# Kernel tuning notes

Hardware: AMD Instinct MI355X
Metric: run time of the kernel (lower is better)

Reference implementation:

```python
import jax, jax.numpy as jnp
import numpy as np

B, N, D = 2, 2048, 1024
H = 16
HD = D // H
C = 4
INTERACTION_BOOST = 0.3
EPS = 1e-6


def _rmsnorm(t, w):
    # t: (B,H,N,HD), w: (HD,)
    var = jnp.mean(t * t, axis=-1, keepdims=True)
    return t * jax.lax.rsqrt(var + EPS) * w


def setup_inputs() -> dict:
    key = jax.random.key(0)
    ks = jax.random.split(key, 8)
    return {
        "x": jax.random.normal(ks[0], (B, N, D), dtype=jnp.float32),
        "character_masks": jax.random.uniform(ks[1], (B, C, N), dtype=jnp.float32),
        "interaction_mask": jax.random.uniform(ks[2], (B, N, N), dtype=jnp.float32),
        "W_qkv": jax.random.normal(ks[3], (3 * D, D), dtype=jnp.float32) * 0.02,
        "W_out": jax.random.normal(ks[4], (D, D), dtype=jnp.float32) * 0.02,
        "q_norm_w": jnp.ones((HD,), dtype=jnp.float32),
        "k_norm_w": jnp.ones((HD,), dtype=jnp.float32),
        "isolation_gate": jax.random.uniform(ks[5], (H,), dtype=jnp.float32),
    }


def reference(x, character_masks, interaction_mask, W_qkv, W_out,
              q_norm_w, k_norm_w, isolation_gate) -> jnp.ndarray:
    b, n, d = x.shape
    h, hd = isolation_gate.shape[0], d // isolation_gate.shape[0]

    qkv = x @ W_qkv.T                       # (B,N,3D)
    q, k, v = jnp.split(qkv, 3, axis=-1)
    def to_heads(t):
        return t.reshape(b, n, h, hd).transpose(0, 2, 1, 3)  # (B,H,N,HD)
    q, k, v = to_heads(q), to_heads(k), to_heads(v)

    q = _rmsnorm(q, q_norm_w)
    k = _rmsnorm(k, k_norm_w)

    scale = hd ** -0.5
    attn = jnp.einsum('bhqd,bhkd->bhqk', q, k) * scale   # (B,H,N,N)

    # isolation bias: same-character co-membership, row-max normalized
    same = jnp.einsum('bcq,bck->bqk', character_masks, character_masks)  # (B,N,N)
    same = same / jnp.clip(jnp.max(same, axis=-1, keepdims=True), 1e-6)
    bias = (same - 0.5) * 2.0 + INTERACTION_BOOST * interaction_mask     # (B,N,N)

    gate = jnp.clip(isolation_gate, 0.0, 1.0)[None, :, None, None]       # (1,H,1,1)
    attn = attn + gate * bias[:, None, :, :] * 3.0

    attn = jax.nn.softmax(attn, axis=-1)
    out = jnp.einsum('bhqk,bhkd->bhqd', attn, v)          # (B,H,N,HD)
    out = out.transpose(0, 2, 1, 3).reshape(b, n, d)      # (B,N,D)
    return out @ W_out.T
```

## Files before the change

### kernel.cpp

```cpp
#include <hip/hip_runtime.h>
#include <math.h>


typedef __attribute__((ext_vector_type(8))) short s8v;
typedef __attribute__((ext_vector_type(4))) short s4v;
typedef __attribute__((ext_vector_type(4))) float f4v;

#define L2E 1.44269504088896340736f

__device__ __forceinline__ unsigned short f2bf(float x) {
    union { float f; unsigned u; } v; v.f = x;
    unsigned r = v.u + 0x7FFF + ((v.u >> 16) & 1);
    return (unsigned short)(r >> 16);
}
__device__ __forceinline__ float bf2f(unsigned short h) {
    union { unsigned u; float f; } v; v.u = ((unsigned)h) << 16;
    return v.f;
}
__device__ __forceinline__ f4v mfma32(s8v a, s8v b, f4v c) {
    return __builtin_amdgcn_mfma_f32_16x16x32_bf16(a, b, c, 0, 0, 0);
}
__device__ __forceinline__ void gl_lds16(const void* g, void* l) {
    __builtin_amdgcn_global_load_lds(
        (const __attribute__((address_space(1))) unsigned*)g,
        (__attribute__((address_space(3))) unsigned*)l, 16, 0, 0);
}
__device__ __forceinline__ float exp2g(float x) {
    float r; asm("v_exp_f32 %0, %1" : "=v"(r) : "v"(x)); return r;
}

__global__ __launch_bounds__(256)
void planes_k(const float* __restrict__ src, short* __restrict__ ph,
              short* __restrict__ pl)
{
    const int i = blockIdx.x * 256 + threadIdx.x;
    float4 f = ((const float4*)src)[i];
    float fa[4] = {f.x, f.y, f.z, f.w};
    s4v h4, l4;
#pragma unroll
    for (int j = 0; j < 4; j++) {
        unsigned short hb = f2bf(fa[j]);
        h4[j] = (short)hb;
        l4[j] = (short)f2bf(fa[j] - bf2f(hb));
    }
    ((s4v*)ph)[i] = h4;
    ((s4v*)pl)[i] = l4;
}

template<int MODE, int NT>
__global__ __launch_bounds__(512, 2)
void gemm2(const short* __restrict__ Ah, const short* __restrict__ Al,
           const short* __restrict__ Bh, const short* __restrict__ Bl,
           short* __restrict__ Qhp, short* __restrict__ Qlp,
           short* __restrict__ Khp, short* __restrict__ Klp,
           short* __restrict__ Vp, float* __restrict__ Cout,
           const float* __restrict__ qw, const float* __restrict__ kw)
{
    extern __shared__ short L[];
    short* sAh = L;
    short* sAl = L + 8192;
    short* sBh = L + 16384;
    short* sBl = L + 24576;

    const int t = threadIdx.x, w = t >> 6, lane = t & 63;
    const int col = lane & 15, quad = lane >> 4;
    const int wm = w >> 1;
    const int wn = w & 1;

    const int srow = t >> 2;
    const int sko  = ((t & 3) ^ (srow & 3)) * 8;
    const int sdst = t * 8;

    int tid = blockIdx.x;
    int m0 = (tid & 31) * 128, n0 = (tid >> 5) * 128;
    const short* agh = Ah + (size_t)(m0 + srow)*1024 + sko;
    const short* agl = Al + (size_t)(m0 + srow)*1024 + sko;
    const short* bgh = Bh + (size_t)(n0 + srow)*1024 + sko;
    const short* bgl = Bl + (size_t)(n0 + srow)*1024 + sko;

    auto stage = [&](int k0, int pp) {
        gl_lds16(agh + k0, &sAh[pp*4096 + sdst]);
        gl_lds16(agl + k0, &sAl[pp*4096 + sdst]);
        gl_lds16(bgh + k0, &sBh[pp*4096 + sdst]);
        gl_lds16(bgl + k0, &sBl[pp*4096 + sdst]);
    };
    stage(0, 0);

    for (int rep = 0; rep < NT; rep++) {
        __syncthreads();

        f4v acc[2][4];
#pragma unroll
        for (int i = 0; i < 2; i++)
#pragma unroll
            for (int j = 0; j < 4; j++) { f4v z = {0.f,0.f,0.f,0.f}; acc[i][j] = z; }

        for (int kt = 0; kt < 32; kt++) {
            const int pp = kt & 1;
            if (kt < 31) stage((kt + 1) * 32, pp ^ 1);

            const int swz = ((quad ^ (col & 3)) << 3);
            s8v bhf[4], blf[4];
#pragma unroll
            for (int j = 0; j < 4; j++) {
                const int boff = pp*4096 + (wn*64 + j*16 + col)*32 + swz;
                bhf[j] = *(const s8v*)&sBh[boff];
                blf[j] = *(const s8v*)&sBl[boff];
            }
#pragma unroll
            for (int i = 0; i < 2; i++) {
                const int aoff = pp*4096 + (wm*32 + i*16 + col)*32 + swz;
                s8v ah = *(const s8v*)&sAh[aoff];
                s8v al = *(const s8v*)&sAl[aoff];
#pragma unroll
                for (int j = 0; j < 4; j++) {
                    acc[i][j] = mfma32(ah, bhf[j], acc[i][j]);
                    acc[i][j] = mfma32(ah, blf[j], acc[i][j]);
                    acc[i][j] = mfma32(al, bhf[j], acc[i][j]);
                }
            }
            __syncthreads();
        }

        const int em0 = m0, en0 = n0;
        if (rep + 1 < NT) {
            tid = blockIdx.x + (rep + 1) * 256;
            m0 = (tid & 31) * 128; n0 = (tid >> 5) * 128;
            agh = Ah + (size_t)(m0 + srow)*1024 + sko;
            agl = Al + (size_t)(m0 + srow)*1024 + sko;
            bgh = Bh + (size_t)(n0 + srow)*1024 + sko;
            bgl = Bl + (size_t)(n0 + srow)*1024 + sko;
            stage(0, 0);
        }

        if (MODE == 0) {
            const int whichW = (en0 + wn*64) >> 10;
            if (whichW < 2) {
                const float* nw = (whichW == 0) ? qw : kw;
                const float sfac = (whichW == 0) ? (0.125f * L2E) : 1.0f;
                float wj[4];
#pragma unroll
                for (int j = 0; j < 4; j++) wj[j] = nw[j*16 + col] * sfac;
#pragma unroll
                for (int i = 0; i < 2; i++)
#pragma unroll
                for (int r = 0; r < 4; r++) {
                    float s2 = acc[i][0][r]*acc[i][0][r] + acc[i][1][r]*acc[i][1][r]
                             + acc[i][2][r]*acc[i][2][r] + acc[i][3][r]*acc[i][3][r];
                    s2 += __shfl_xor(s2, 1);
                    s2 += __shfl_xor(s2, 2);
                    s2 += __shfl_xor(s2, 4);
                    s2 += __shfl_xor(s2, 8);
                    const float scn = rsqrtf(s2*(1.0f/64.0f) + 1e-6f);
#pragma unroll
                    for (int j = 0; j < 4; j++) acc[i][j][r] *= scn*wj[j];
                }
            }
#pragma unroll
            for (int i = 0; i < 2; i++)
#pragma unroll
            for (int j = 0; j < 4; j++) {
                const int gcol = en0 + wn*64 + j*16 + col;
                const int which = gcol >> 10;
                const int hh = (gcol >> 6) & 15;
                const int hd = gcol & 63;
                const int grow0 = em0 + wm*32 + i*16 + quad*4;
                const int b = grow0 >> 11, nn0 = grow0 & 2047;
                if (which == 2) {
                    s4v hv;
#pragma unroll
                    for (int r = 0; r < 4; r++) hv[r] = (short)f2bf(acc[i][j][r]);
                    const int nswz = (nn0 & ~60) | ((nn0 & 12) << 2) | ((nn0 & 48) >> 2);
                    *(s4v*)&Vp[((size_t)(b*16 + hh)*64 + hd)*2048 + nswz] = hv;
                } else {
                    short* Hp = (which == 0) ? Qhp : Khp;
                    short* Lp = (which == 0) ? Qlp : Klp;
                    const size_t base = ((size_t)(b*16 + hh)*2048 + nn0)*64 + hd;
#pragma unroll
                    for (int r = 0; r < 4; r++) {
                        const float v = acc[i][j][r];
                        const unsigned short hb = f2bf(v);
                        union { float f; unsigned u; } rr; rr.f = v - bf2f(hb);
                        Hp[base + (size_t)r*64] = (short)hb;
                        Lp[base + (size_t)r*64] = (short)(rr.u >> 16);
                    }
                }
            }
        } else {
#pragma unroll
            for (int i = 0; i < 2; i++)
#pragma unroll
            for (int j = 0; j < 4; j++) {
                const int gcol = en0 + wn*64 + j*16 + col;
#pragma unroll
                for (int r = 0; r < 4; r++) {
                    const int grow = em0 + wm*32 + i*16 + quad*4 + r;
                    Cout[(size_t)grow*1024 + gcol] = acc[i][j][r];
                }
            }
        }
    }
}

__global__ __launch_bounds__(256)
void rowscale_k(const float* __restrict__ cm, float* __restrict__ rs)
{
    __shared__ float cms[4][2048];
    const int b  = blockIdx.x >> 5;
    const int qt = blockIdx.x & 31;
    const float* base = cm + (size_t)b * 4 * 2048;
    for (int i = threadIdx.x; i < 2048; i += 256) {
        cms[0][i] = base[i];
        cms[1][i] = base[2048 + i];
        cms[2][i] = base[4096 + i];
        cms[3][i] = base[6144 + i];
    }
    __syncthreads();
    const int q    = qt * 64 + (threadIdx.x >> 2);
    const int part = threadIdx.x & 3;
    const float a0 = cms[0][q], a1 = cms[1][q], a2 = cms[2][q], a3 = cms[3][q];
    float mx = 0.f;
    for (int i = 0; i < 512; i++) {
        const int k = part + 4 * i;
        float d = a0*cms[0][k] + a1*cms[1][k] + a2*cms[2][k] + a3*cms[3][k];
        mx = fmaxf(mx, d);
    }
    mx = fmaxf(mx, __shfl_xor(mx, 1));
    mx = fmaxf(mx, __shfl_xor(mx, 2));
    if (part == 0) rs[b * 2048 + q] = 1.0f / fmaxf(mx, 1e-6f);
}

__global__ __launch_bounds__(256)
void bias_pre(const float* __restrict__ cm, const float* __restrict__ im,
              const float* __restrict__ rs, float* __restrict__ Bias2)
{
    const int bid = blockIdx.x;
    const int qq = bid & 15;
    const int kt = (bid >> 4) & 31;
    const int b  = bid >> 9;

    __shared__ float cmk[4][64];
    const int t = threadIdx.x;
    const int k0 = kt * 64;
    cmk[t >> 6][t & 63] = cm[(size_t)b*8192 + (t >> 6)*2048 + k0 + (t & 63)];
    __syncthreads();

    const int klane = t & 15;
    const int qrow  = t >> 4;
    const int kk = k0 + klane*4;
    const int kg = kk >> 2;
    float ck[4][4];
#pragma unroll
    for (int c = 0; c < 4; c++)
#pragma unroll
        for (int j = 0; j < 4; j++) ck[c][j] = cmk[c][klane*4 + j];

    const float* cmb = cm + (size_t)b * 8192;
    const float kS = 3.0f * L2E;
    for (int it = 0; it < 8; it++) {
        const int q = qq*128 + it*16 + qrow;
        float4 imv = *(const float4*)(im + ((size_t)b*2048 + q)*2048 + kk);
        const float rsq = rs[b*2048 + q];
        const float c0 = cmb[q], c1 = cmb[2048+q], c2 = cmb[4096+q], c3 = cmb[6144+q];
        float o[4];
        float iv[4] = {imv.x, imv.y, imv.z, imv.w};
#pragma unroll
        for (int j = 0; j < 4; j++) {
            float same = c0*ck[0][j] + c1*ck[1][j] + c2*ck[2][j] + c3*ck[3][j];
            o[j] = ((same*rsq - 0.5f)*2.0f + 0.3f*iv[j]) * kS;
        }
        *(float4*)(Bias2 + (((size_t)b*512 + kg)*2048 + q)*4) =
            make_float4(o[0], o[1], o[2], o[3]);
    }
}

__global__ __launch_bounds__(256, 2)
void attn_mfma(const short* __restrict__ Qhp, const short* __restrict__ Qlp,
               const short* __restrict__ Khg, const short* __restrict__ Klg,
               const short* __restrict__ VtG, const float* __restrict__ Bias2,
               const float* __restrict__ gate, short* __restrict__ Oh,
               short* __restrict__ Ol)
{
    const int bid = blockIdx.x;
    const int h  = bid & 15;
    const int qt = (bid >> 4) & 15;
    const int b  = bid >> 8;

    __shared__ __align__(16) short Kbuf[2][2][64*64];
    __shared__ __align__(16) short Vbuf[2][64*64];

    const int t    = threadIdx.x;
    const int w    = t >> 6;
    const int lane = t & 63;
    const int col  = lane & 15;
    const int quad = lane >> 4;

    const size_t headoff = ((size_t)(b*16 + h)) * 2048 * 64;
    const int qb = qt*128 + w*32;

    s8v qfh[2][2], qfl[2][2];
#pragma unroll
    for (int n = 0; n < 2; n++)
#pragma unroll
    for (int c = 0; c < 2; c++) {
        const size_t off = headoff + (size_t)(qb + n*16 + col)*64 + c*32 + quad*8;
        qfh[n][c] = *(const s8v*)(Qhp + off);
        qfl[n][c] = *(const s8v*)(Qlp + off);
    }

    const float g = fminf(fmaxf(gate[h], 0.f), 1.f);

    s8v ones8;
#pragma unroll
    for (int j = 0; j < 8; j++) ones8[j] = (short)0x3F80;

    f4v liacc[2];
    f4v Oa[4][2];
    {
        f4v z = {0.f,0.f,0.f,0.f};
        liacc[0] = z; liacc[1] = z;
#pragma unroll
        for (int dt = 0; dt < 4; dt++)
#pragma unroll
            for (int n = 0; n < 2; n++) Oa[dt][n] = z;
    }

    const short* ksrc_h = Khg + headoff + (size_t)(w*8 + (lane>>3))*64
                          + ((lane&7) ^ (lane>>3))*8;
    const short* ksrc_l = Klg + headoff + (size_t)(w*8 + (lane>>3))*64
                          + ((lane&7) ^ (lane>>3))*8;
    const short* vsrcT = VtG + headoff + (size_t)(w*8 + (lane>>3))*2048
                          + ((lane&7) ^ (lane>>3))*8;

    const float* bptr[2];
#pragma unroll
    for (int n = 0; n < 2; n++)
        bptr[n] = Bias2 + (((size_t)b*512 + quad)*2048 + qb + n*16 + col)*4;

    auto dma = [&](int kbase, int pp) {
#pragma unroll
        for (int j = 0; j < 2; j++) {
            gl_lds16(ksrc_h + (size_t)kbase*64 + j*2048, &Kbuf[pp][0][(j*4 + w)*512]);
            gl_lds16(ksrc_l + (size_t)kbase*64 + j*2048, &Kbuf[pp][1][(j*4 + w)*512]);
        }
#pragma unroll
        for (int cc = 0; cc < 2; cc++)
            gl_lds16(vsrcT + (size_t)(kbase + cc*65536), &Vbuf[pp][cc*2048 + w*512]);
    };

    float4 biasA[4][2], biasB[4][2];

    dma(0, 0);
#pragma unroll
    for (int s = 0; s < 4; s++)
#pragma unroll
    for (int n = 0; n < 2; n++)
        biasA[s][n] = *(const float4*)(bptr[n] + (size_t)s*4*8192);
    __syncthreads();

    auto tile = [&](int kt, int pp, float4 (&BC)[4][2], float4 (&BN)[4][2]) {
        const int kbase = kt * 64;
        const bool pre = kt < 31;
        if (pre) {
            dma(kbase + 64, pp ^ 1);
#pragma unroll
            for (int s = 0; s < 4; s++)
#pragma unroll
            for (int n = 0; n < 2; n++)
                BN[s][n] = *(const float4*)(bptr[n] +
                    ((size_t)((kbase >> 2) + 16) + s*4)*8192);
        }

        f4v S[4][2];
#pragma unroll
        for (int s = 0; s < 4; s++)
#pragma unroll
            for (int n = 0; n < 2; n++) { f4v z = {0.f,0.f,0.f,0.f}; S[s][n] = z; }
#pragma unroll
        for (int s = 0; s < 4; s++)
#pragma unroll
        for (int c = 0; c < 2; c++) {
            const int koff = (s*16 + col)*64 + (((c*4 + quad) ^ (col & 7)) << 3);
            s8v kh = *(const s8v*)&Kbuf[pp][0][koff];
            s8v kl = *(const s8v*)&Kbuf[pp][1][koff];
#pragma unroll
            for (int n = 0; n < 2; n++) {
                S[s][n] = mfma32(kh, qfh[n][c], S[s][n]);
                S[s][n] = mfma32(kh, qfl[n][c], S[s][n]);
                S[s][n] = mfma32(kl, qfh[n][c], S[s][n]);
            }
        }

        s8v ph8[2][2];
#pragma unroll
        for (int n = 0; n < 2; n++) {
            union { unsigned uu[4]; s8v v; } pk0, pk1;
#pragma unroll
            for (int s = 0; s < 4; s++) {
                const float bb[4] = {BC[s][n].x, BC[s][n].y, BC[s][n].z, BC[s][n].w};
                const float p0 = exp2g(fmaf(bb[0], g, S[s][n][0]));
                const float p1 = exp2g(fmaf(bb[1], g, S[s][n][1]));
                const float p2 = exp2g(fmaf(bb[2], g, S[s][n][2]));
                const float p3 = exp2g(fmaf(bb[3], g, S[s][n][3]));
                unsigned u01, u23;
                asm("v_cvt_pk_bf16_f32 %0, %1, %2" : "=v"(u01) : "v"(p0), "v"(p1));
                asm("v_cvt_pk_bf16_f32 %0, %1, %2" : "=v"(u23) : "v"(p2), "v"(p3));
                if (s < 2) { pk0.uu[s*2] = u01;     pk0.uu[s*2 + 1] = u23; }
                else       { pk1.uu[(s-2)*2] = u01; pk1.uu[(s-2)*2 + 1] = u23; }
            }
            ph8[n][0] = pk0.v;
            ph8[n][1] = pk1.v;
        }

#pragma unroll
        for (int n = 0; n < 2; n++)
#pragma unroll
        for (int m = 0; m < 2; m++)
            liacc[n] = mfma32(ones8, ph8[n][m], liacc[n]);

#pragma unroll
        for (int dt = 0; dt < 4; dt++) {
            const int vrow = (dt*16 + col)*64;
            s8v v0 = *(const s8v*)&Vbuf[pp][vrow + ((((quad*2)    ) ^ (col & 7)) << 3)];
            s8v v1 = *(const s8v*)&Vbuf[pp][vrow + ((((quad*2) + 1) ^ (col & 7)) << 3)];
#pragma unroll
            for (int n = 0; n < 2; n++) {
                Oa[dt][n] = mfma32(v0, ph8[n][0], Oa[dt][n]);
                Oa[dt][n] = mfma32(v1, ph8[n][1], Oa[dt][n]);
            }
        }

        if (pre) __syncthreads();
    };

    for (int kt = 0; kt < 32; kt += 2) {
        tile(kt,     0, biasA, biasB);
        tile(kt + 1, 1, biasB, biasA);
    }

#pragma unroll
    for (int n = 0; n < 2; n++) {
        const float inv = 1.0f / liacc[n][0];
        const size_t row = (size_t)b*2048 + qb + n*16 + col;
#pragma unroll
        for (int dt = 0; dt < 4; dt++) {
            s4v hv, lv;
#pragma unroll
            for (int r = 0; r < 4; r++) {
                float y = Oa[dt][n][r] * inv;
                unsigned short hb = f2bf(y);
                hv[r] = (short)hb;
                union { float f; unsigned u; } rr; rr.f = y - bf2f(hb);
                lv[r] = (short)(rr.u >> 16);
            }
            const size_t o = row*1024 + h*64 + dt*16 + quad*4;
            *(s4v*)&Oh[o] = hv;
            *(s4v*)&Ol[o] = lv;
        }
    }
}

extern "C" void kernel_launch(void* const* d_in, const int* in_sizes, int n_in,
                              void* d_out, int out_size, void* d_ws, size_t ws_size,
                              hipStream_t stream)
{
    const float* x    = (const float*)d_in[0];
    const float* cm   = (const float*)d_in[1];
    const float* im   = (const float*)d_in[2];
    const float* Wqkv = (const float*)d_in[3];
    const float* Wout = (const float*)d_in[4];
    const float* qw   = (const float*)d_in[5];
    const float* kw   = (const float*)d_in[6];
    const float* gate = (const float*)d_in[7];
    float* out = (float*)d_out;

    char* ws = (char*)d_ws;
    short* qhp = (short*)(ws);
    short* qlp = (short*)(ws +  8388608);
    short* khp = (short*)(ws + 16777216);
    short* klp = (short*)(ws + 25165824);
    short* vp  = (short*)(ws + 33554432);
    short* oh  = (short*)(ws + 41943040);
    short* ol  = (short*)(ws + 50331648);
    short* woh = (short*)(ws + 58720256);
    short* wol = (short*)(ws + 60817408);
    float* rsb = (float*)(ws + 62914560);
    char*  U   = ws + 62930944;
    short* xh  = (short*)(U);
    short* xl  = (short*)(U +  8388608);
    short* wqh = (short*)(U + 16777216);
    short* wql = (short*)(U + 23068672);
    float* bias2 = (float*)(U);

    static bool lds_init = false;
    if (!lds_init) {
        hipFuncSetAttribute((const void*)&gemm2<0,3>,
                            hipFuncAttributeMaxDynamicSharedMemorySize, 65536);
        hipFuncSetAttribute((const void*)&gemm2<1,1>,
                            hipFuncAttributeMaxDynamicSharedMemorySize, 65536);
        lds_init = true;
    }

    planes_k<<<4096, 256, 0, stream>>>(x,    xh,  xl);
    planes_k<<<3072, 256, 0, stream>>>(Wqkv, wqh, wql);
    planes_k<<<1024, 256, 0, stream>>>(Wout, woh, wol);
    gemm2<0,3><<<256, 512, 65536, stream>>>(xh, xl, wqh, wql,
        qhp, qlp, khp, klp, vp, nullptr, qw, kw);
    rowscale_k<<<64, 256, 0, stream>>>(cm, rsb);
    bias_pre<<<1024, 256, 0, stream>>>(cm, im, rsb, bias2);
    attn_mfma<<<512, 256, 0, stream>>>(qhp, qlp, khp, klp, vp, bias2, gate,
                                       oh, ol);
    gemm2<1,1><<<256, 512, 65536, stream>>>(oh, ol, woh, wol,
        nullptr, nullptr, nullptr, nullptr, nullptr, out, nullptr, nullptr);
}
```

Before: 351.0 us.

## Use a dedicated 256x192-tile QKV GEMM with cross-wave split RMSNorm reduction

Replaces the persistent 128x128-tile QKV projection, where each block looped over three tiles, with a new kernel that gives each block one 256x192 output tile over a 16x16 grid. The larger tile raises reuse of the staged split-bf16 operands from LDS and removes the per-tile restaging loop. Because 192-wide tiles split a 64-wide head across two waves, partial sums of squares for RMSNorm are exchanged through LDS with an extra barrier. It also uses more LDS per block and more accumulator registers, which may lower occupancy; the output GEMM kernel is simplified to a single-tile version.

```diff
diff --git a/kernel.cpp b/kernel.cpp
--- a/kernel.cpp
+++ b/kernel.cpp
@@ -47,14 +47,189 @@
     ((s4v*)pl)[i] = l4;
 }
 
+__global__ __launch_bounds__(512, 2)
+void gemm_qkv2(const short* __restrict__ Ah, const short* __restrict__ Al,
+               const short* __restrict__ Bh, const short* __restrict__ Bl,
+               short* __restrict__ Qhp, short* __restrict__ Qlp,
+               short* __restrict__ Khp, short* __restrict__ Klp,
+               short* __restrict__ Vp,
+               const float* __restrict__ qw, const float* __restrict__ kw)
+{
+    extern __shared__ short L[];
+    short* sAh = L;
+    short* sAl = L + 16384;
+    short* sBh = L + 32768;
+    short* sBl = L + 45056;
+
+    const int t = threadIdx.x, w = t >> 6, lane = t & 63;
+    const int col = lane & 15, quad = lane >> 4;
+    const int wm = w >> 1;
+    const int wn = w & 1;
+    const int m0 = blockIdx.y * 256, n0 = blockIdx.x * 192;
+
+    f4v acc[4][6];
+#pragma unroll
+    for (int i = 0; i < 4; i++)
+#pragma unroll
+        for (int j = 0; j < 6; j++) { f4v z = {0.f,0.f,0.f,0.f}; acc[i][j] = z; }
+
+    const int ca0 = t, ca1 = t + 512;
+    const int cb0 = t, cb1 = t + 384;
+    const bool doB = t < 384;
+    #define SRCOFF(c, base, rbase) ((size_t)((rbase) + ((c) >> 2))*1024 \
+                                    + (((c) & 3) ^ (((c) >> 2) & 3))*8)
+
+    auto stage = [&](int k0, int pp) {
+        gl_lds16(Ah + SRCOFF(ca0, 0, m0) + k0, &sAh[pp*8192 + ca0*8]);
+        gl_lds16(Ah + SRCOFF(ca1, 0, m0) + k0, &sAh[pp*8192 + ca1*8]);
+        gl_lds16(Al + SRCOFF(ca0, 0, m0) + k0, &sAl[pp*8192 + ca0*8]);
+        gl_lds16(Al + SRCOFF(ca1, 0, m0) + k0, &sAl[pp*8192 + ca1*8]);
+        if (doB) {
+            gl_lds16(Bh + SRCOFF(cb0, 0, n0) + k0, &sBh[pp*6144 + cb0*8]);
+            gl_lds16(Bh + SRCOFF(cb1, 0, n0) + k0, &sBh[pp*6144 + cb1*8]);
+            gl_lds16(Bl + SRCOFF(cb0, 0, n0) + k0, &sBl[pp*6144 + cb0*8]);
+            gl_lds16(Bl + SRCOFF(cb1, 0, n0) + k0, &sBl[pp*6144 + cb1*8]);
+        }
+    };
+
+    stage(0, 0);
+    __syncthreads();
+
+    for (int kt = 0; kt < 32; kt++) {
+        const int pp = kt & 1;
+        if (kt < 31) stage((kt + 1) * 32, pp ^ 1);
+
+        const int swz = ((quad ^ (col & 3)) << 3);
+        s8v bhf[6], blf[6];
+#pragma unroll
+        for (int j = 0; j < 6; j++) {
+            const int boff = pp*6144 + (wn*96 + j*16 + col)*32 + swz;
+            bhf[j] = *(const s8v*)&sBh[boff];
+            blf[j] = *(const s8v*)&sBl[boff];
+        }
+#pragma unroll
+        for (int i = 0; i < 4; i++) {
+            const int aoff = pp*8192 + (wm*64 + i*16 + col)*32 + swz;
+            s8v ah = *(const s8v*)&sAh[aoff];
+            s8v al = *(const s8v*)&sAl[aoff];
+#pragma unroll
+            for (int j = 0; j < 6; j++) {
+                acc[i][j] = mfma32(ah, bhf[j], acc[i][j]);
+                acc[i][j] = mfma32(ah, blf[j], acc[i][j]);
+                acc[i][j] = mfma32(al, bhf[j], acc[i][j]);
+            }
+        }
+        __syncthreads();
+    }
+
+    const int whichF = (n0 + wn*128) >> 10;
+    const int whichB = (n0 + 64) >> 10;
+    const int j0  = 2*wn;
+    const int jb0 = 4 - 4*wn;
+
+    if (whichF < 2) {
+        const float* nw = (whichF == 0) ? qw : kw;
+        const float sfac = (whichF == 0) ? (0.125f * L2E) : 1.0f;
+        float wj[4];
+#pragma unroll
+        for (int j = 0; j < 4; j++) wj[j] = nw[j*16 + col] * sfac;
+#pragma unroll
+        for (int i = 0; i < 4; i++)
+#pragma unroll
+        for (int r = 0; r < 4; r++) {
+            float s2 = acc[i][j0+0][r]*acc[i][j0+0][r]
+                     + acc[i][j0+1][r]*acc[i][j0+1][r]
+                     + acc[i][j0+2][r]*acc[i][j0+2][r]
+                     + acc[i][j0+3][r]*acc[i][j0+3][r];
+            s2 += __shfl_xor(s2, 1);
+            s2 += __shfl_xor(s2, 2);
+            s2 += __shfl_xor(s2, 4);
+            s2 += __shfl_xor(s2, 8);
+            const float scn = rsqrtf(s2*(1.0f/64.0f) + 1e-6f);
+#pragma unroll
+            for (int j = 0; j < 4; j++) acc[i][j0+j][r] *= scn*wj[j];
+        }
+    }
+
+    float pB[4][4];
+    float* pb = (float*)L;
+    if (whichB < 2) {
+#pragma unroll
+        for (int i = 0; i < 4; i++)
+#pragma unroll
+        for (int r = 0; r < 4; r++) {
+            float s2 = acc[i][jb0][r]*acc[i][jb0][r]
+                     + acc[i][jb0+1][r]*acc[i][jb0+1][r];
+            s2 += __shfl_xor(s2, 1);
+            s2 += __shfl_xor(s2, 2);
+            s2 += __shfl_xor(s2, 4);
+            s2 += __shfl_xor(s2, 8);
+            pB[i][r] = s2;
+        }
+        if (col == 0) {
+#pragma unroll
+            for (int i = 0; i < 4; i++)
+#pragma unroll
+            for (int r = 0; r < 4; r++)
+                pb[wn*256 + wm*64 + i*16 + quad*4 + r] = pB[i][r];
+        }
+    }
+    __syncthreads();
+    if (whichB < 2) {
+        const float* nw = (whichB == 0) ? qw : kw;
+        const float sfac = (whichB == 0) ? (0.125f * L2E) : 1.0f;
+        float wj[2];
+#pragma unroll
+        for (int j = 0; j < 2; j++) wj[j] = nw[(wn*2 + j)*16 + col] * sfac;
+#pragma unroll
+        for (int i = 0; i < 4; i++)
+#pragma unroll
+        for (int r = 0; r < 4; r++) {
+            const float s2 = pB[i][r]
+                + pb[(wn^1)*256 + wm*64 + i*16 + quad*4 + r];
+            const float scn = rsqrtf(s2*(1.0f/64.0f) + 1e-6f);
+            acc[i][jb0  ][r] *= scn*wj[0];
+            acc[i][jb0+1][r] *= scn*wj[1];
+        }
+    }
+
+#pragma unroll
+    for (int i = 0; i < 4; i++)
+#pragma unroll
+    for (int j = 0; j < 6; j++) {
+        const int gcol = n0 + wn*96 + j*16 + col;
+        const int which = gcol >> 10;
+        const int hh = (gcol >> 6) & 15;
+        const int hd = gcol & 63;
+        const int grow0 = m0 + wm*64 + i*16 + quad*4;
+        const int b = grow0 >> 11, nn0 = grow0 & 2047;
+        if (which == 2) {
+            s4v hv;
+#pragma unroll
+            for (int r = 0; r < 4; r++) hv[r] = (short)f2bf(acc[i][j][r]);
+            const int nswz = (nn0 & ~60) | ((nn0 & 12) << 2) | ((nn0 & 48) >> 2);
+            *(s4v*)&Vp[((size_t)(b*16 + hh)*64 + hd)*2048 + nswz] = hv;
+        } else {
+            short* Hp = (which == 0) ? Qhp : Khp;
+            short* Lp = (which == 0) ? Qlp : Klp;
+            const size_t base = ((size_t)(b*16 + hh)*2048 + nn0)*64 + hd;
+#pragma unroll
+            for (int r = 0; r < 4; r++) {
+                const float v = acc[i][j][r];
+                const unsigned short hb = f2bf(v);
+                union { float f; unsigned u; } rr; rr.f = v - bf2f(hb);
+                Hp[base + (size_t)r*64] = (short)hb;
+                Lp[base + (size_t)r*64] = (short)(rr.u >> 16);
+            }
+        }
+    }
+}
+
 template<int MODE, int NT>
 __global__ __launch_bounds__(512, 2)
 void gemm2(const short* __restrict__ Ah, const short* __restrict__ Al,
            const short* __restrict__ Bh, const short* __restrict__ Bl,
-           short* __restrict__ Qhp, short* __restrict__ Qlp,
-           short* __restrict__ Khp, short* __restrict__ Klp,
-           short* __restrict__ Vp, float* __restrict__ Cout,
-           const float* __restrict__ qw, const float* __restrict__ kw)
+           float* __restrict__ Cout)
 {
     extern __shared__ short L[];
     short* sAh = L;
@@ -85,119 +260,50 @@
         gl_lds16(bgl + k0, &sBl[pp*4096 + sdst]);
     };
     stage(0, 0);
-
-    for (int rep = 0; rep < NT; rep++) {
+    __syncthreads();
+
+    f4v acc[2][4];
+#pragma unroll
+    for (int i = 0; i < 2; i++)
+#pragma unroll
+        for (int j = 0; j < 4; j++) { f4v z = {0.f,0.f,0.f,0.f}; acc[i][j] = z; }
+
+    for (int kt = 0; kt < 32; kt++) {
+        const int pp = kt & 1;
+        if (kt < 31) stage((kt + 1) * 32, pp ^ 1);
+
+        const int swz = ((quad ^ (col & 3)) << 3);
+        s8v bhf[4], blf[4];
+#pragma unroll
+        for (int j = 0; j < 4; j++) {
+            const int boff = pp*4096 + (wn*64 + j*16 + col)*32 + swz;
+            bhf[j] = *(const s8v*)&sBh[boff];
+            blf[j] = *(const s8v*)&sBl[boff];
+        }
+#pragma unroll
+        for (int i = 0; i < 2; i++) {
+            const int aoff = pp*4096 + (wm*32 + i*16 + col)*32 + swz;
+            s8v ah = *(const s8v*)&sAh[aoff];
+            s8v al = *(const s8v*)&sAl[aoff];
+#pragma unroll
+            for (int j = 0; j < 4; j++) {
+                acc[i][j] = mfma32(ah, bhf[j], acc[i][j]);
+                acc[i][j] = mfma32(ah, blf[j], acc[i][j]);
+                acc[i][j] = mfma32(al, bhf[j], acc[i][j]);
+            }
+        }
         __syncthreads();
-
-        f4v acc[2][4];
-#pragma unroll
-        for (int i = 0; i < 2; i++)
-#pragma unroll
-            for (int j = 0; j < 4; j++) { f4v z = {0.f,0.f,0.f,0.f}; acc[i][j] = z; }
-
-        for (int kt = 0; kt < 32; kt++) {
-            const int pp = kt & 1;
-            if (kt < 31) stage((kt + 1) * 32, pp ^ 1);
-
-            const int swz = ((quad ^ (col & 3)) << 3);
-            s8v bhf[4], blf[4];
-#pragma unroll
-            for (int j = 0; j < 4; j++) {
-                const int boff = pp*4096 + (wn*64 + j*16 + col)*32 + swz;
-                bhf[j] = *(const s8v*)&sBh[boff];
-                blf[j] = *(const s8v*)&sBl[boff];
-            }
-#pragma unroll
-            for (int i = 0; i < 2; i++) {
-                const int aoff = pp*4096 + (wm*32 + i*16 + col)*32 + swz;
-                s8v ah = *(const s8v*)&sAh[aoff];
-                s8v al = *(const s8v*)&sAl[aoff];
-#pragma unroll
-                for (int j = 0; j < 4; j++) {
-                    acc[i][j] = mfma32(ah, bhf[j], acc[i][j]);
-                    acc[i][j] = mfma32(ah, blf[j], acc[i][j]);
-                    acc[i][j] = mfma32(al, bhf[j], acc[i][j]);
-                }
-            }
-            __syncthreads();
-        }
-
-        const int em0 = m0, en0 = n0;
-        if (rep + 1 < NT) {
-            tid = blockIdx.x + (rep + 1) * 256;
-            m0 = (tid & 31) * 128; n0 = (tid >> 5) * 128;
-            agh = Ah + (size_t)(m0 + srow)*1024 + sko;
-            agl = Al + (size_t)(m0 + srow)*1024 + sko;
-            bgh = Bh + (size_t)(n0 + srow)*1024 + sko;
-            bgl = Bl + (size_t)(n0 + srow)*1024 + sko;
-            stage(0, 0);
-        }
-
-        if (MODE == 0) {
-            const int whichW = (en0 + wn*64) >> 10;
-            if (whichW < 2) {
-                const float* nw = (whichW == 0) ? qw : kw;
-                const float sfac = (whichW == 0) ? (0.125f * L2E) : 1.0f;
-                float wj[4];
-#pragma unroll
-                for (int j = 0; j < 4; j++) wj[j] = nw[j*16 + col] * sfac;
-#pragma unroll
-                for (int i = 0; i < 2; i++)
-#pragma unroll
-                for (int r = 0; r < 4; r++) {
-                    float s2 = acc[i][0][r]*acc[i][0][r] + acc[i][1][r]*acc[i][1][r]
-                             + acc[i][2][r]*acc[i][2][r] + acc[i][3][r]*acc[i][3][r];
-                    s2 += __shfl_xor(s2, 1);
-                    s2 += __shfl_xor(s2, 2);
-                    s2 += __shfl_xor(s2, 4);
-                    s2 += __shfl_xor(s2, 8);
-                    const float scn = rsqrtf(s2*(1.0f/64.0f) + 1e-6f);
-#pragma unroll
-                    for (int j = 0; j < 4; j++) acc[i][j][r] *= scn*wj[j];
-                }
-            }
-#pragma unroll
-            for (int i = 0; i < 2; i++)
-#pragma unroll
-            for (int j = 0; j < 4; j++) {
-                const int gcol = en0 + wn*64 + j*16 + col;
-                const int which = gcol >> 10;
-                const int hh = (gcol >> 6) & 15;
-                const int hd = gcol & 63;
-                const int grow0 = em0 + wm*32 + i*16 + quad*4;
-                const int b = grow0 >> 11, nn0 = grow0 & 2047;
-                if (which == 2) {
-                    s4v hv;
-#pragma unroll
-                    for (int r = 0; r < 4; r++) hv[r] = (short)f2bf(acc[i][j][r]);
-                    const int nswz = (nn0 & ~60) | ((nn0 & 12) << 2) | ((nn0 & 48) >> 2);
-                    *(s4v*)&Vp[((size_t)(b*16 + hh)*64 + hd)*2048 + nswz] = hv;
-                } else {
-                    short* Hp = (which == 0) ? Qhp : Khp;
-                    short* Lp = (which == 0) ? Qlp : Klp;
-                    const size_t base = ((size_t)(b*16 + hh)*2048 + nn0)*64 + hd;
-#pragma unroll
-                    for (int r = 0; r < 4; r++) {
-                        const float v = acc[i][j][r];
-                        const unsigned short hb = f2bf(v);
-                        union { float f; unsigned u; } rr; rr.f = v - bf2f(hb);
-                        Hp[base + (size_t)r*64] = (short)hb;
-                        Lp[base + (size_t)r*64] = (short)(rr.u >> 16);
-                    }
-                }
-            }
-        } else {
-#pragma unroll
-            for (int i = 0; i < 2; i++)
-#pragma unroll
-            for (int j = 0; j < 4; j++) {
-                const int gcol = en0 + wn*64 + j*16 + col;
-#pragma unroll
-                for (int r = 0; r < 4; r++) {
-                    const int grow = em0 + wm*32 + i*16 + quad*4 + r;
-                    Cout[(size_t)grow*1024 + gcol] = acc[i][j][r];
-                }
-            }
+    }
+
+#pragma unroll
+    for (int i = 0; i < 2; i++)
+#pragma unroll
+    for (int j = 0; j < 4; j++) {
+        const int gcol = n0 + wn*64 + j*16 + col;
+#pragma unroll
+        for (int r = 0; r < 4; r++) {
+            const int grow = m0 + wm*32 + i*16 + quad*4 + r;
+            Cout[(size_t)grow*1024 + gcol] = acc[i][j][r];
         }
     }
 }
@@ -494,8 +600,8 @@
 
     static bool lds_init = false;
     if (!lds_init) {
-        hipFuncSetAttribute((const void*)&gemm2<0,3>,
-                            hipFuncAttributeMaxDynamicSharedMemorySize, 65536);
+        hipFuncSetAttribute((const void*)&gemm_qkv2,
+                            hipFuncAttributeMaxDynamicSharedMemorySize, 114688);
         hipFuncSetAttribute((const void*)&gemm2<1,1>,
                             hipFuncAttributeMaxDynamicSharedMemorySize, 65536);
         lds_init = true;
@@ -504,12 +610,11 @@
     planes_k<<<4096, 256, 0, stream>>>(x,    xh,  xl);
     planes_k<<<3072, 256, 0, stream>>>(Wqkv, wqh, wql);
     planes_k<<<1024, 256, 0, stream>>>(Wout, woh, wol);
-    gemm2<0,3><<<256, 512, 65536, stream>>>(xh, xl, wqh, wql,
-        qhp, qlp, khp, klp, vp, nullptr, qw, kw);
+    gemm_qkv2<<<dim3(16, 16), 512, 114688, stream>>>(xh, xl, wqh, wql,
+        qhp, qlp, khp, klp, vp, qw, kw);
     rowscale_k<<<64, 256, 0, stream>>>(cm, rsb);
     bias_pre<<<1024, 256, 0, stream>>>(cm, im, rsb, bias2);
     attn_mfma<<<512, 256, 0, stream>>>(qhp, qlp, khp, klp, vp, bias2, gate,
                                        oh, ol);
-    gemm2<1,1><<<256, 512, 65536, stream>>>(oh, ol, woh, wol,
-        nullptr, nullptr, nullptr, nullptr, nullptr, out, nullptr, nullptr);
-}
+    gemm2<1,1><<<256, 512, 65536, stream>>>(oh, ol, woh, wol, out);
+}
```

New measurement: 782.7 us. +123.0%, slower.
